# Kernel tuning notes

Hardware: AMD Instinct MI355X
Metric: run time of the kernel (lower is better)

Reference implementation:

```python
import jax, jax.numpy as jnp
import numpy as np

B, S, D, H = 4, 2048, 512, 8
EPS = 1e-5

def _layer_norm(x, gamma, beta):
    mu = jnp.mean(x, axis=-1, keepdims=True)
    var = jnp.mean(jnp.square(x - mu), axis=-1, keepdims=True)
    return (x - mu) * jax.lax.rsqrt(var + EPS) * gamma + beta

def setup_inputs() -> dict:
    key = jax.random.key(0)
    ks = jax.random.split(key, 6)
    sc = 1.0 / np.sqrt(D)
    return {
        "seq_k": jax.random.normal(ks[0], (B, S, D), jnp.float32),
        "seq_q": jax.random.normal(ks[1], (B, S, D), jnp.float32),
        "seq_v": jax.random.normal(ks[2], (B, S, D), jnp.float32),
        "W1": jax.random.normal(ks[3], (D, D), jnp.float32) * sc,
        "W2": jax.random.normal(ks[4], (D, D), jnp.float32) * sc,
        "W3": jax.random.normal(ks[5], (D, D), jnp.float32) * sc,
        "gamma": jnp.ones((D,), jnp.float32),
        "beta": jnp.zeros((D,), jnp.float32),
    }

def reference(seq_k, seq_q, seq_v, W1, W2, W3, gamma, beta):
    # is_layer_norm=True: pre-LN on values; seq_v_value is the normed v
    v_in = _layer_norm(seq_v, gamma, beta)
    # nn.Linear(bias=False): y = x @ W^T
    q = seq_q @ W1.T
    k = seq_k @ W2.T
    v = v_in @ W3.T
    hd = D // H
    q = q.reshape(B, S, H, hd).transpose(0, 2, 1, 3)  # b h s d
    k = k.reshape(B, S, H, hd).transpose(0, 2, 1, 3)
    v = v.reshape(B, S, H, hd).transpose(0, 2, 1, 3)
    # faithful quirk: scores = K @ Q^T, unscaled
    scores = jnp.einsum("bhid,bhjd->bhij", k, q)  # b h s s
    attn = jax.nn.softmax(scores, axis=-1)
    out = jnp.einsum("bhij,bhjd->bhid", attn, v)  # b h s d
    out = out.transpose(0, 2, 1, 3).reshape(B, S, D)
    out = out + v_in                 # is_residual=True
    return _layer_norm(out, gamma, beta)  # final LN
```

## Files before the change

### kernel.cpp

```cpp
#include <hip/hip_runtime.h>
#include <math.h>

#define BB 4
#define SS 2048
#define DD 512
#define HH 8
#define HD 64
#define NTOK (BB*SS)
#define EPS 1e-5f
#define NE ((size_t)NTOK * DD)
#define WN ((size_t)DD * DD)
#define LOG2E 1.4426950408889634f

typedef _Float16 half8v __attribute__((ext_vector_type(8)));
typedef _Float16 half4v __attribute__((ext_vector_type(4)));
typedef _Float16 half2v __attribute__((ext_vector_type(2)));
typedef float f32x4 __attribute__((ext_vector_type(4)));

__device__ __forceinline__ float fast_exp2(float x) {
#if __has_builtin(__builtin_amdgcn_exp2f)
    return __builtin_amdgcn_exp2f(x);
#else
    return __expf(x * 0.6931471805599453f);
#endif
}

__device__ __forceinline__ half2v pack2(float a, float b) {
    return __builtin_bit_cast(half2v, __builtin_amdgcn_cvt_pkrtz(a, b));
}

__device__ __forceinline__ half4v pack4(float a, float b, float c, float d) {
    half2v lo = pack2(a, b);
    half2v hi = pack2(c, d);
    half4v r; r[0] = lo[0]; r[1] = lo[1]; r[2] = hi[0]; r[3] = hi[1];
    return r;
}

__device__ __forceinline__ void gload_lds16(const void* g, void* l) {
    __builtin_amdgcn_global_load_lds(
        (const __attribute__((address_space(1))) unsigned int*)g,
        (__attribute__((address_space(3))) unsigned int*)l, 16, 0, 0);
}

__global__ __launch_bounds__(256) void ln_kernel(const float* __restrict__ x,
                                                 const float* __restrict__ res,
                                                 const float* __restrict__ gamma,
                                                 const float* __restrict__ beta,
                                                 float* __restrict__ y) {
    int row = blockIdx.x;
    const float* xr = x + (size_t)row * DD;
    int t = threadIdx.x;
    float2 v = ((const float2*)xr)[t];
    {
        float2 r = ((const float2*)(res + (size_t)row * DD))[t];
        v.x += r.x; v.y += r.y;
    }
    float s = v.x + v.y;
    float ss = v.x * v.x + v.y * v.y;
    #pragma unroll
    for (int off = 32; off; off >>= 1) {
        s  += __shfl_down(s,  off);
        ss += __shfl_down(ss, off);
    }
    __shared__ float ws0[4], ws1[4];
    int wid = t >> 6, lane = t & 63;
    if (lane == 0) { ws0[wid] = s; ws1[wid] = ss; }
    __syncthreads();
    __shared__ float mu_s, rstd_s;
    if (t == 0) {
        float S0 = ws0[0] + ws0[1] + ws0[2] + ws0[3];
        float S1 = ws1[0] + ws1[1] + ws1[2] + ws1[3];
        float mu = S0 * (1.0f / DD);
        float var = S1 * (1.0f / DD) - mu * mu;
        mu_s = mu;
        rstd_s = rsqrtf(var + EPS);
    }
    __syncthreads();
    float mu = mu_s, rstd = rstd_s;
    float2 g = ((const float2*)gamma)[t];
    float2 bb = ((const float2*)beta)[t];
    float2 o;
    o.x = (v.x - mu) * rstd * g.x + bb.x;
    o.y = (v.y - mu) * rstd * g.y + bb.y;
    ((float2*)(y + (size_t)row * DD))[t] = o;
}

__global__ __launch_bounds__(256) void prep_kernel(const float* __restrict__ seq_v,
                                                   const float* __restrict__ seq_q,
                                                   const float* __restrict__ seq_k,
                                                   const float* __restrict__ W1,
                                                   const float* __restrict__ W2,
                                                   const float* __restrict__ W3,
                                                   const float* __restrict__ gamma,
                                                   const float* __restrict__ beta,
                                                   float* __restrict__ v_in,
                                                   _Float16* __restrict__ v16,
                                                   _Float16* __restrict__ qk16,
                                                   _Float16* __restrict__ w16) {
    int bid = blockIdx.x;
    int t = threadIdx.x;
    if (bid < NTOK) {
        int row = bid;
        float2 v = ((const float2*)(seq_v + (size_t)row * DD))[t];
        float s = v.x + v.y;
        float ss = v.x * v.x + v.y * v.y;
        #pragma unroll
        for (int off = 32; off; off >>= 1) {
            s  += __shfl_down(s,  off);
            ss += __shfl_down(ss, off);
        }
        __shared__ float ws0[4], ws1[4];
        int wid = t >> 6, lane = t & 63;
        if (lane == 0) { ws0[wid] = s; ws1[wid] = ss; }
        __syncthreads();
        __shared__ float mu_s, rstd_s;
        if (t == 0) {
            float S0 = ws0[0] + ws0[1] + ws0[2] + ws0[3];
            float S1 = ws1[0] + ws1[1] + ws1[2] + ws1[3];
            float mu = S0 * (1.0f / DD);
            float var = S1 * (1.0f / DD) - mu * mu;
            mu_s = mu;
            rstd_s = rsqrtf(var + EPS);
        }
        __syncthreads();
        float mu = mu_s, rstd = rstd_s;
        float2 g = ((const float2*)gamma)[t];
        float2 bb = ((const float2*)beta)[t];
        float2 o;
        o.x = (v.x - mu) * rstd * g.x + bb.x;
        o.y = (v.y - mu) * rstd * g.y + bb.y;
        ((float2*)(v_in + (size_t)row * DD))[t] = o;
        *(half2v*)&v16[(size_t)row * DD + 2 * t] = pack2(o.x, o.y);
    } else if (bid < 2 * NTOK) {
        size_t i = ((size_t)(bid - NTOK) * 256 + t) * 4;
        const float* src = (i < NE) ? (seq_q + i) : (seq_k + (i - NE));
        float4 v = *(const float4*)src;
        *(half4v*)(qk16 + i) = pack4(v.x, v.y, v.z, v.w);
    } else {
        size_t i = ((size_t)(bid - 2 * NTOK) * 256 + t) * 4;
        const float* src; float sc;
        if (i < WN)          { src = W1 + i;            sc = LOG2E; }
        else if (i < 2 * WN) { src = W2 + (i - WN);     sc = 1.0f; }
        else                 { src = W3 + (i - 2 * WN); sc = 1.0f; }
        float4 v = *(const float4*)src;
        *(half4v*)(w16 + i) = pack4(v.x * sc, v.y * sc, v.z * sc, v.w * sc);
    }
}

#define GBM 128
#define GBN 128
#define GBK 64
__global__ __launch_bounds__(256) void gemm_mfma(const _Float16* __restrict__ Aall,
                                                 const _Float16* __restrict__ Wall,
                                                 _Float16* __restrict__ Call,
                                                 _Float16* __restrict__ vtOut) {
    __shared__ __align__(16) _Float16 As[GBM * GBK];
    __shared__ __align__(16) _Float16 Ws[GBN * GBK];
    int z = blockIdx.z;
    bool isv = (z == 2);
    const _Float16* A = Aall + (size_t)z * NE;
    const _Float16* W = Wall + (size_t)z * WN;
    int t = threadIdx.x, w = t >> 6, lane = t & 63, q = lane >> 4, ln = lane & 15;
    int lrow = lane >> 3, lseg = lane & 7;
    int m0 = blockIdx.y * GBM, n0 = blockIdx.x * GBN;
    int wm = w & 1, wn = w >> 1;
    f32x4 acc[4][4];
    #pragma unroll
    for (int mt = 0; mt < 4; ++mt)
        #pragma unroll
        for (int nt = 0; nt < 4; ++nt)
            acc[mt][nt] = (f32x4){0.f, 0.f, 0.f, 0.f};

    int gs = lseg ^ lrow;
    for (int k0 = 0; k0 < DD; k0 += GBK) {
        #pragma unroll
        for (int p = 0; p < 4; ++p) {
            int r = w * 32 + p * 8 + lrow;
            gload_lds16(A + (size_t)(m0 + r) * DD + k0 + gs * 8,
                        As + (size_t)(w * 32 + p * 8) * GBK);
            gload_lds16(W + (size_t)(n0 + r) * DD + k0 + gs * 8,
                        Ws + (size_t)(w * 32 + p * 8) * GBK);
        }
        __syncthreads();
        #pragma unroll
        for (int kk = 0; kk < 2; ++kk) {
            int ch = ((4 * kk + q) ^ (ln & 7)) * 8;
            half8v af[4], wf[4];
            #pragma unroll
            for (int mt = 0; mt < 4; ++mt)
                af[mt] = *(half8v*)&As[(wm * 64 + mt * 16 + ln) * GBK + ch];
            #pragma unroll
            for (int nt = 0; nt < 4; ++nt)
                wf[nt] = *(half8v*)&Ws[(wn * 64 + nt * 16 + ln) * GBK + ch];
            if (!isv) {
                #pragma unroll
                for (int mt = 0; mt < 4; ++mt)
                    #pragma unroll
                    for (int nt = 0; nt < 4; ++nt)
                        acc[mt][nt] = __builtin_amdgcn_mfma_f32_16x16x32_f16(
                            wf[nt], af[mt], acc[mt][nt], 0, 0, 0);
            } else {
                #pragma unroll
                for (int mt = 0; mt < 4; ++mt)
                    #pragma unroll
                    for (int nt = 0; nt < 4; ++nt)
                        acc[mt][nt] = __builtin_amdgcn_mfma_f32_16x16x32_f16(
                            af[mt], wf[nt], acc[mt][nt], 0, 0, 0);
            }
        }
        __syncthreads();
    }
    if (!isv) {
        _Float16* C = Call + (size_t)z * NE;
        #pragma unroll
        for (int mt = 0; mt < 4; ++mt) {
            int m = m0 + wm * 64 + mt * 16 + ln;
            int b = m >> 11, s = m & (SS - 1);
            #pragma unroll
            for (int nt = 0; nt < 4; ++nt) {
                int nb = n0 + wn * 64 + nt * 16 + q * 4;
                int h = nb >> 6, d0 = nb & 63;
                half4v pv = pack4(acc[mt][nt][0], acc[mt][nt][1],
                                  acc[mt][nt][2], acc[mt][nt][3]);
                *(half4v*)&C[((size_t)(b * HH + h) * SS + s) * HD + d0] = pv;
            }
        }
    } else {
        #pragma unroll
        for (int mt = 0; mt < 4; ++mt) {
            int mb = m0 + wm * 64 + mt * 16 + q * 4;
            int b = mb >> 11, s0 = mb & (SS - 1);
            #pragma unroll
            for (int nt = 0; nt < 4; ++nt) {
                int n = n0 + wn * 64 + nt * 16 + ln;
                int h = n >> 6, d = n & 63;
                half4v pv = pack4(acc[mt][nt][0], acc[mt][nt][1],
                                  acc[mt][nt][2], acc[mt][nt][3]);
                *(half4v*)&vtOut[((size_t)(b * HH + h) * HD + d) * SS + s0] = pv;
            }
        }
    }
}

#define AI 128
#define AJ 64
__global__ __launch_bounds__(512, 4) void attn_mfma(const _Float16* __restrict__ qh,
                                                    const _Float16* __restrict__ kh,
                                                    const _Float16* __restrict__ vt,
                                                    float* __restrict__ out) {
    __shared__ __align__(16) _Float16 Qt[3][AJ * HD];
    __shared__ __align__(16) _Float16 Vs[2][HD * AJ];
    __shared__ __align__(16) _Float16 Ps[AI * AJ];
    int t = threadIdx.x, w = t >> 6, lane = t & 63, q = lane >> 4, ln = lane & 15;
    int wg = blockIdx.x;
    int slot = wg >> 3;
    int bh = (wg & 7) * 4 + (slot >> 4);
    int i0 = (slot & 15) * AI;
    int b = bh >> 3, h = bh & 7;
    const _Float16* Kb = kh + (size_t)bh * SS * HD;
    const _Float16* Qb = qh + (size_t)bh * SS * HD;
    const _Float16* Vb = vt + (size_t)bh * HD * SS;

    half8v kf[2];
    #pragma unroll
    for (int kk = 0; kk < 2; ++kk)
        kf[kk] = *(const half8v*)&Kb[(size_t)(i0 + w * 16 + ln) * HD + kk * 32 + q * 8];

    f32x4 oacc[4], lacc;
    float m_run = -3.0e38f;
    lacc = (f32x4){0.f, 0.f, 0.f, 0.f};
    #pragma unroll
    for (int mtd = 0; mtd < 4; ++mtd) oacc[mtd] = (f32x4){0.f, 0.f, 0.f, 0.f};
    half8v ones;
    #pragma unroll
    for (int e = 0; e < 8; ++e) ones[e] = (_Float16)1.0f;
    const f32x4 zf = (f32x4){0.f, 0.f, 0.f, 0.f};

    int sr = t >> 3;
    int sc = t & 7;
    int ssw = sc ^ (sr & 7);

    gload_lds16(Qb + (size_t)sr * HD + ssw * 8, &Qt[0][(size_t)w * 512]);
    gload_lds16(Vb + (size_t)sr * SS + ssw * 8, &Vs[0][(size_t)w * 512]);
    __syncthreads();
    gload_lds16(Qb + (size_t)(AJ + sr) * HD + ssw * 8, &Qt[1][(size_t)w * 512]);

    f32x4 sacc[4];
    #pragma unroll
    for (int mt = 0; mt < 4; ++mt) {
        half8v qf = *(half8v*)&Qt[0][(mt * 16 + ln) * HD + (q ^ (ln & 7)) * 8];
        sacc[mt] = __builtin_amdgcn_mfma_f32_16x16x32_f16(qf, kf[0], zf, 0, 0, 0);
    }
    #pragma unroll
    for (int mt = 0; mt < 4; ++mt) {
        half8v qf = *(half8v*)&Qt[0][(mt * 16 + ln) * HD + ((4 + q) ^ (ln & 7)) * 8];
        sacc[mt] = __builtin_amdgcn_mfma_f32_16x16x32_f16(qf, kf[1], sacc[mt], 0, 0, 0);
    }

    int rb = 1, sb = 2, vb = 0;
    const int NITER = SS / AJ;
    for (int jt = 0; jt < NITER; ++jt) {
        __syncthreads();

        if (jt + 2 < NITER)
            gload_lds16(Qb + (size_t)((jt + 2) * AJ + sr) * HD + ssw * 8,
                        &Qt[sb][(size_t)w * 512]);
        if (jt + 1 < NITER)
            gload_lds16(Vb + (size_t)sr * SS + (jt + 1) * AJ + ssw * 8,
                        &Vs[vb ^ 1][(size_t)w * 512]);

        f32x4 snx[4] = {zf, zf, zf, zf};
        if (jt + 1 < NITER) {
            __builtin_amdgcn_s_setprio(1);
            #pragma unroll
            for (int mt = 0; mt < 4; ++mt) {
                half8v qf = *(half8v*)&Qt[rb][(mt * 16 + ln) * HD + (q ^ (ln & 7)) * 8];
                snx[mt] = __builtin_amdgcn_mfma_f32_16x16x32_f16(qf, kf[0], zf, 0, 0, 0);
            }
            #pragma unroll
            for (int mt = 0; mt < 4; ++mt) {
                half8v qf = *(half8v*)&Qt[rb][(mt * 16 + ln) * HD + ((4 + q) ^ (ln & 7)) * 8];
                snx[mt] = __builtin_amdgcn_mfma_f32_16x16x32_f16(qf, kf[1], snx[mt], 0, 0, 0);
            }
            __builtin_amdgcn_s_setprio(0);
        }

        float mx = fmaxf(fmaxf(sacc[0][0], sacc[0][1]), fmaxf(sacc[0][2], sacc[0][3]));
        #pragma unroll
        for (int mt = 1; mt < 4; ++mt) {
            float m2 = fmaxf(fmaxf(sacc[mt][0], sacc[mt][1]),
                             fmaxf(sacc[mt][2], sacc[mt][3]));
            mx = fmaxf(mx, m2);
        }
        mx = fmaxf(mx, __shfl_xor(mx, 16));
        mx = fmaxf(mx, __shfl_xor(mx, 32));
        if (__any(mx > m_run + 7.0f)) {
            float mn = fmaxf(m_run, mx);
            float a = fast_exp2(m_run - mn);
            lacc *= a;
            #pragma unroll
            for (int mtd = 0; mtd < 4; ++mtd) oacc[mtd] *= a;
            m_run = mn;
        }
        int rp = w * 16 + ln;
        #pragma unroll
        for (int mt = 0; mt < 4; ++mt) {
            float p0 = fast_exp2(sacc[mt][0] - m_run);
            float p1 = fast_exp2(sacc[mt][1] - m_run);
            float p2 = fast_exp2(sacc[mt][2] - m_run);
            float p3 = fast_exp2(sacc[mt][3] - m_run);
            int cw = mt * 2 + (q >> 1);
            int pos = cw ^ (ln & 7);
            *(half4v*)&Ps[(size_t)rp * AJ + pos * 8 + (q & 1) * 4] =
                pack4(p0, p1, p2, p3);
        }

        __builtin_amdgcn_s_setprio(1);
        #pragma unroll
        for (int ks = 0; ks < 2; ++ks) {
            int pos = ((ks * 4 + q) ^ (ln & 7)) * 8;
            half8v pf = *(half8v*)&Ps[(size_t)(w * 16 + ln) * AJ + pos];
            lacc = __builtin_amdgcn_mfma_f32_16x16x32_f16(ones, pf, lacc, 0, 0, 0);
            #pragma unroll
            for (int mtd = 0; mtd < 4; ++mtd) {
                half8v vf = *(half8v*)&Vs[vb][(size_t)(mtd * 16 + ln) * AJ + pos];
                oacc[mtd] = __builtin_amdgcn_mfma_f32_16x16x32_f16(vf, pf, oacc[mtd], 0, 0, 0);
            }
        }
        __builtin_amdgcn_s_setprio(0);

        #pragma unroll
        for (int mt = 0; mt < 4; ++mt) sacc[mt] = snx[mt];
        rb = (rb == 2) ? 0 : rb + 1;
        sb = (sb == 2) ? 0 : sb + 1;
        vb ^= 1;
    }

    float inv = 1.0f / lacc[0];
    int i = i0 + w * 16 + ln;
    #pragma unroll
    for (int mtd = 0; mtd < 4; ++mtd) {
        float4 o;
        o.x = oacc[mtd][0] * inv;
        o.y = oacc[mtd][1] * inv;
        o.z = oacc[mtd][2] * inv;
        o.w = oacc[mtd][3] * inv;
        *(float4*)&out[(size_t)(b * SS + i) * DD + h * HD + mtd * 16 + q * 4] = o;
    }
}

extern "C" void kernel_launch(void* const* d_in, const int* in_sizes, int n_in,
                              void* d_out, int out_size, void* d_ws, size_t ws_size,
                              hipStream_t stream) {
    const float* seq_k = (const float*)d_in[0];
    const float* seq_q = (const float*)d_in[1];
    const float* seq_v = (const float*)d_in[2];
    const float* W1    = (const float*)d_in[3];
    const float* W2    = (const float*)d_in[4];
    const float* W3    = (const float*)d_in[5];
    const float* gamma = (const float*)d_in[6];
    const float* beta  = (const float*)d_in[7];
    float* out = (float*)d_out;

    const size_t MB = 1024 * 1024;
    char* w8 = (char*)d_ws;
    float*    v_in = (float*)w8;
    _Float16* a16  = (_Float16*)(w8 + 16 * MB);
    _Float16* w16  = (_Float16*)(w8 + 40 * MB);
    _Float16* qh   = (_Float16*)(w8 + 48 * MB);
    _Float16* vt   = (_Float16*)(w8 + 64 * MB);
    float*    ao   = (float*)(w8 + 16 * MB);

    _Float16* q16 = a16;
    _Float16* v16 = a16 + 2 * NE;
    _Float16* kh  = qh + NE;

    hipLaunchKernelGGL(prep_kernel, dim3(2 * NTOK + 768), dim3(256), 0, stream,
                       seq_v, seq_q, seq_k, W1, W2, W3, gamma, beta,
                       v_in, v16, q16, w16);
    hipLaunchKernelGGL(gemm_mfma, dim3(DD / GBN, NTOK / GBM, 3), dim3(256), 0, stream,
                       a16, w16, qh, vt);
    hipLaunchKernelGGL(attn_mfma, dim3((SS / AI) * BB * HH), dim3(512), 0, stream,
                       qh, kh, vt, ao);
    hipLaunchKernelGGL(ln_kernel, dim3(NTOK), dim3(256), 0, stream,
                       ao, v_in, gamma, beta, out);
}
```

Measured before the change: 201.7 us.

## Stage GEMM epilogue through LDS and simplify attention Q/V double-buffering

The GEMM epilogue now writes accumulators into a swizzled shared-memory tile, then reads them back to emit 16-byte coalesced global stores for both the head-major Q/K layout and the transposed V layout. The attention kernel drops the software-pipelined score computation, where S for the next tile was computed ahead with a triple-buffered Q. It now uses plain double buffering, computing scores for the current tile each iteration. This cuts LDS use and register pressure (no snx array), possibly raising occupancy, but gives up overlapping the QK MFMA with the softmax of the previous tile.

Result: no change. 197.9 us (-1.9%).

```diff
diff --git a/kernel.cpp b/kernel.cpp
--- a/kernel.cpp
+++ b/kernel.cpp
@@ -154,8 +154,9 @@
                                                  const _Float16* __restrict__ Wall,
                                                  _Float16* __restrict__ Call,
                                                  _Float16* __restrict__ vtOut) {
-    __shared__ __align__(16) _Float16 As[GBM * GBK];
-    __shared__ __align__(16) _Float16 Ws[GBN * GBK];
+    __shared__ __align__(16) _Float16 smem[GBM * GBN];
+    _Float16* As = smem;
+    _Float16* Ws = smem + (size_t)GBM * GBK;
     int z = blockIdx.z;
     bool isv = (z == 2);
     const _Float16* A = Aall + (size_t)z * NE;
@@ -210,34 +211,56 @@
         }
         __syncthreads();
     }
+
+    if (!isv) {
+        #pragma unroll
+        for (int mt = 0; mt < 4; ++mt) {
+            int mloc = wm * 64 + mt * 16 + ln;
+            #pragma unroll
+            for (int nt = 0; nt < 4; ++nt) {
+                int nloc = wn * 64 + nt * 16 + q * 4;
+                int cs = (nloc >> 3) ^ (mloc & 7);
+                char* p = (char*)smem + mloc * 256 + cs * 16 + (nloc & 7) * 2;
+                *(half4v*)p = pack4(acc[mt][nt][0], acc[mt][nt][1],
+                                    acc[mt][nt][2], acc[mt][nt][3]);
+            }
+        }
+    } else {
+        #pragma unroll
+        for (int nt = 0; nt < 4; ++nt) {
+            int dloc = wn * 64 + nt * 16 + ln;
+            #pragma unroll
+            for (int mt = 0; mt < 4; ++mt) {
+                int sloc = wm * 64 + mt * 16 + q * 4;
+                int cs = (sloc >> 3) ^ (dloc & 7);
+                char* p = (char*)smem + dloc * 256 + cs * 16 + (sloc & 7) * 2;
+                *(half4v*)p = pack4(acc[mt][nt][0], acc[mt][nt][1],
+                                    acc[mt][nt][2], acc[mt][nt][3]);
+            }
+        }
+    }
+    __syncthreads();
+    int bq = m0 >> 11, sbase = m0 & (SS - 1);
     if (!isv) {
         _Float16* C = Call + (size_t)z * NE;
         #pragma unroll
-        for (int mt = 0; mt < 4; ++mt) {
-            int m = m0 + wm * 64 + mt * 16 + ln;
-            int b = m >> 11, s = m & (SS - 1);
-            #pragma unroll
-            for (int nt = 0; nt < 4; ++nt) {
-                int nb = n0 + wn * 64 + nt * 16 + q * 4;
-                int h = nb >> 6, d0 = nb & 63;
-                half4v pv = pack4(acc[mt][nt][0], acc[mt][nt][1],
-                                  acc[mt][nt][2], acc[mt][nt][3]);
-                *(half4v*)&C[((size_t)(b * HH + h) * SS + s) * HD + d0] = pv;
-            }
+        for (int p = 0; p < 8; ++p) {
+            int id = p * 256 + t;
+            int r = id >> 4, c = id & 15;
+            half8v vv = *(half8v*)((char*)smem + r * 256 + ((c ^ (r & 7)) * 16));
+            int n = n0 + c * 8;
+            int h = n >> 6, d0 = n & 63;
+            *(half8v*)&C[((size_t)(bq * HH + h) * SS + (sbase + r)) * HD + d0] = vv;
         }
     } else {
         #pragma unroll
-        for (int mt = 0; mt < 4; ++mt) {
-            int mb = m0 + wm * 64 + mt * 16 + q * 4;
-            int b = mb >> 11, s0 = mb & (SS - 1);
-            #pragma unroll
-            for (int nt = 0; nt < 4; ++nt) {
-                int n = n0 + wn * 64 + nt * 16 + ln;
-                int h = n >> 6, d = n & 63;
-                half4v pv = pack4(acc[mt][nt][0], acc[mt][nt][1],
-                                  acc[mt][nt][2], acc[mt][nt][3]);
-                *(half4v*)&vtOut[((size_t)(b * HH + h) * HD + d) * SS + s0] = pv;
-            }
+        for (int p = 0; p < 8; ++p) {
+            int id = p * 256 + t;
+            int r = id >> 4, c = id & 15;
+            half8v vv = *(half8v*)((char*)smem + r * 256 + ((c ^ (r & 7)) * 16));
+            int d = n0 + r;
+            int h = d >> 6, dd = d & 63;
+            *(half8v*)&vtOut[((size_t)(bq * HH + h) * HD + dd) * SS + sbase + c * 8] = vv;
         }
     }
 }
@@ -248,7 +271,7 @@
                                                     const _Float16* __restrict__ kh,
                                                     const _Float16* __restrict__ vt,
                                                     float* __restrict__ out) {
-    __shared__ __align__(16) _Float16 Qt[3][AJ * HD];
+    __shared__ __align__(16) _Float16 Qt[2][AJ * HD];
     __shared__ __align__(16) _Float16 Vs[2][HD * AJ];
     __shared__ __align__(16) _Float16 Ps[AI * AJ];
     int t = threadIdx.x, w = t >> 6, lane = t & 63, q = lane >> 4, ln = lane & 15;
@@ -282,48 +305,31 @@
 
     gload_lds16(Qb + (size_t)sr * HD + ssw * 8, &Qt[0][(size_t)w * 512]);
     gload_lds16(Vb + (size_t)sr * SS + ssw * 8, &Vs[0][(size_t)w * 512]);
-    __syncthreads();
-    gload_lds16(Qb + (size_t)(AJ + sr) * HD + ssw * 8, &Qt[1][(size_t)w * 512]);
-
-    f32x4 sacc[4];
-    #pragma unroll
-    for (int mt = 0; mt < 4; ++mt) {
-        half8v qf = *(half8v*)&Qt[0][(mt * 16 + ln) * HD + (q ^ (ln & 7)) * 8];
-        sacc[mt] = __builtin_amdgcn_mfma_f32_16x16x32_f16(qf, kf[0], zf, 0, 0, 0);
-    }
-    #pragma unroll
-    for (int mt = 0; mt < 4; ++mt) {
-        half8v qf = *(half8v*)&Qt[0][(mt * 16 + ln) * HD + ((4 + q) ^ (ln & 7)) * 8];
-        sacc[mt] = __builtin_amdgcn_mfma_f32_16x16x32_f16(qf, kf[1], sacc[mt], 0, 0, 0);
-    }
-
-    int rb = 1, sb = 2, vb = 0;
+
     const int NITER = SS / AJ;
     for (int jt = 0; jt < NITER; ++jt) {
+        int cur = jt & 1;
         __syncthreads();
 
-        if (jt + 2 < NITER)
-            gload_lds16(Qb + (size_t)((jt + 2) * AJ + sr) * HD + ssw * 8,
-                        &Qt[sb][(size_t)w * 512]);
-        if (jt + 1 < NITER)
-            gload_lds16(Vb + (size_t)sr * SS + (jt + 1) * AJ + ssw * 8,
-                        &Vs[vb ^ 1][(size_t)w * 512]);
-
-        f32x4 snx[4] = {zf, zf, zf, zf};
         if (jt + 1 < NITER) {
-            __builtin_amdgcn_s_setprio(1);
-            #pragma unroll
-            for (int mt = 0; mt < 4; ++mt) {
-                half8v qf = *(half8v*)&Qt[rb][(mt * 16 + ln) * HD + (q ^ (ln & 7)) * 8];
-                snx[mt] = __builtin_amdgcn_mfma_f32_16x16x32_f16(qf, kf[0], zf, 0, 0, 0);
-            }
-            #pragma unroll
-            for (int mt = 0; mt < 4; ++mt) {
-                half8v qf = *(half8v*)&Qt[rb][(mt * 16 + ln) * HD + ((4 + q) ^ (ln & 7)) * 8];
-                snx[mt] = __builtin_amdgcn_mfma_f32_16x16x32_f16(qf, kf[1], snx[mt], 0, 0, 0);
-            }
-            __builtin_amdgcn_s_setprio(0);
-        }
+            int j1 = (jt + 1) * AJ;
+            gload_lds16(Qb + (size_t)(j1 + sr) * HD + ssw * 8, &Qt[cur ^ 1][(size_t)w * 512]);
+            gload_lds16(Vb + (size_t)sr * SS + j1 + ssw * 8,   &Vs[cur ^ 1][(size_t)w * 512]);
+        }
+
+        f32x4 sacc[4];
+        __builtin_amdgcn_s_setprio(1);
+        #pragma unroll
+        for (int mt = 0; mt < 4; ++mt) {
+            half8v qf = *(half8v*)&Qt[cur][(mt * 16 + ln) * HD + (q ^ (ln & 7)) * 8];
+            sacc[mt] = __builtin_amdgcn_mfma_f32_16x16x32_f16(qf, kf[0], zf, 0, 0, 0);
+        }
+        #pragma unroll
+        for (int mt = 0; mt < 4; ++mt) {
+            half8v qf = *(half8v*)&Qt[cur][(mt * 16 + ln) * HD + ((4 + q) ^ (ln & 7)) * 8];
+            sacc[mt] = __builtin_amdgcn_mfma_f32_16x16x32_f16(qf, kf[1], sacc[mt], 0, 0, 0);
+        }
+        __builtin_amdgcn_s_setprio(0);
 
         float mx = fmaxf(fmaxf(sacc[0][0], sacc[0][1]), fmaxf(sacc[0][2], sacc[0][3]));
         #pragma unroll
@@ -342,6 +348,7 @@
             for (int mtd = 0; mtd < 4; ++mtd) oacc[mtd] *= a;
             m_run = mn;
         }
+
         int rp = w * 16 + ln;
         #pragma unroll
         for (int mt = 0; mt < 4; ++mt) {
@@ -363,17 +370,11 @@
             lacc = __builtin_amdgcn_mfma_f32_16x16x32_f16(ones, pf, lacc, 0, 0, 0);
             #pragma unroll
             for (int mtd = 0; mtd < 4; ++mtd) {
-                half8v vf = *(half8v*)&Vs[vb][(size_t)(mtd * 16 + ln) * AJ + pos];
+                half8v vf = *(half8v*)&Vs[cur][(size_t)(mtd * 16 + ln) * AJ + pos];
                 oacc[mtd] = __builtin_amdgcn_mfma_f32_16x16x32_f16(vf, pf, oacc[mtd], 0, 0, 0);
             }
         }
         __builtin_amdgcn_s_setprio(0);
-
-        #pragma unroll
-        for (int mt = 0; mt < 4; ++mt) sacc[mt] = snx[mt];
-        rb = (rb == 2) ? 0 : rb + 1;
-        sb = (sb == 2) ? 0 : sb + 1;
-        vb ^= 1;
     }
 
     float inv = 1.0f / lacc[0];
```
